# Performance work log

Measured on AMD Instinct MI355X. Metric: run time of the kernel, lower is better.

The kernel has to match this reference:

```python
import jax, jax.numpy as jnp
import numpy as np

N = 50000      # ncount
L = 4          # number of wavelet scales
E = 1600000    # nnz per sparse wavelet matrix
C_IN = 128
C_OUT = 128


def setup_inputs() -> dict:
    key = jax.random.key(0)
    ks = jax.random.split(key, 7)
    return {
        "phi_indices": jax.random.randint(ks[0], (L, 2, E), 0, N, dtype=jnp.int32),
        "phi_values": jax.random.uniform(ks[1], (L, E), dtype=jnp.float32),
        "phi_inverse_indices": jax.random.randint(ks[2], (L, 2, E), 0, N, dtype=jnp.int32),
        "phi_inverse_values": jax.random.uniform(ks[3], (L, E), dtype=jnp.float32),
        "features": jax.random.normal(ks[4], (N, L, C_IN), dtype=jnp.float32),
        "weight_matrix": jax.random.normal(ks[5], (C_IN, C_OUT), dtype=jnp.float32) * (6.0 / (C_IN + C_OUT)) ** 0.5,
        "diagonal_weight_filter": jax.random.uniform(ks[6], (N,), dtype=jnp.float32, minval=0.9, maxval=1.1),
    }


def _spmm(idx, vals, X):
    # sparse [N,N] (COO rows=idx[0], cols=idx[1]) @ dense X [N,C]
    row, col = idx[0], idx[1]
    return jax.ops.segment_sum(vals[:, None] * X[col], row, num_segments=N)


def reference(phi_indices, phi_values, phi_inverse_indices, phi_inverse_values,
              features, weight_matrix, diagonal_weight_filter):
    # Original: (phi_i @ diag(theta) @ phi_inv_i) @ (features[:,i,:] @ W)
    # Applied right-to-left via associativity -> three streaming spmm-style ops,
    # never materializing the N x N product matrix.
    def per_scale(p_idx, p_val, pi_idx, pi_val, feat_i):
        y = feat_i @ weight_matrix                 # [N, C_OUT]
        y = _spmm(pi_idx, pi_val, y)               # phi_inverse @ y
        y = y * diagonal_weight_filter[:, None]    # diag(theta) @ y
        return _spmm(p_idx, p_val, y)              # phi @ y

    feats_lf = jnp.moveaxis(features, 1, 0)        # [L, N, C_IN]
    out = jax.vmap(per_scale)(phi_indices, phi_values,
                              phi_inverse_indices, phi_inverse_values, feats_lf)
    return jnp.moveaxis(out, 0, 1)                 # [N, L, C_OUT]
```

## Files before the change

### kernel.cpp

```cpp
#include <hip/hip_runtime.h>

#define N_NODES 50000
#define L_SCALES 4
#define E_NNZ 1600000
#define C 128
#define NL (N_NODES * L_SCALES)

#define ELL_W 64
#define OVF_CAP 8192

#define RPB 16
#define NB (N_NODES / RPB)
#define NSUB 8
#define SCAP 112
#define GROUP 4
#define BT_STRIDE 16

#define SEG_SHIFT 12
#define NSEG 13

__global__ __launch_bounds__(256) void gemm_all(
    const float* __restrict__ feat,
    const float* __restrict__ W,
    float* __restrict__ Y)
{
    __shared__ float As[16][132];
    __shared__ float Ws[16][128];

    int t  = threadIdx.x;
    int ty = t >> 4;
    int tx = t & 15;
    size_t r0 = (size_t)blockIdx.x * 128;

    float acc[8][8];
    #pragma unroll
    for (int i = 0; i < 8; ++i)
        #pragma unroll
        for (int j = 0; j < 8; ++j) acc[i][j] = 0.f;

    for (int kt = 0; kt < C; kt += 16) {
        __syncthreads();
        #pragma unroll
        for (int jj = 0; jj < 2; ++jj) {
            int q = t + 256 * jj;
            int row = q >> 2, pc = q & 3;
            size_t r = r0 + row;
            float4 f = (r < (size_t)NL) ? ((const float4*)(feat + r * C + kt))[pc]
                                        : make_float4(0.f, 0.f, 0.f, 0.f);
            As[pc * 4 + 0][row] = f.x;
            As[pc * 4 + 1][row] = f.y;
            As[pc * 4 + 2][row] = f.z;
            As[pc * 4 + 3][row] = f.w;
            int kr = q >> 5, wpc = q & 31;
            ((float4*)&Ws[kr][0])[wpc] = ((const float4*)(W + (size_t)(kt + kr) * C))[wpc];
        }
        __syncthreads();

        #pragma unroll
        for (int kk = 0; kk < 16; ++kk) {
            float4 a0 = *(const float4*)&As[kk][ty * 8];
            float4 a1 = *(const float4*)&As[kk][ty * 8 + 4];
            float4 w0 = *(const float4*)&Ws[kk][tx * 4];
            float4 w1 = *(const float4*)&Ws[kk][64 + tx * 4];
            float a[8] = {a0.x, a0.y, a0.z, a0.w, a1.x, a1.y, a1.z, a1.w};
            float w[8] = {w0.x, w0.y, w0.z, w0.w, w1.x, w1.y, w1.z, w1.w};
            #pragma unroll
            for (int i = 0; i < 8; ++i)
                #pragma unroll
                for (int j = 0; j < 8; ++j)
                    acc[i][j] = fmaf(a[i], w[j], acc[i][j]);
        }
    }

    #pragma unroll
    for (int i = 0; i < 8; ++i) {
        size_t r = r0 + ty * 8 + i;
        if (r < (size_t)NL) {
            float* orow = Y + r * C;
            *(float4*)(orow + tx * 4)      = make_float4(acc[i][0], acc[i][1], acc[i][2], acc[i][3]);
            *(float4*)(orow + 64 + tx * 4) = make_float4(acc[i][4], acc[i][5], acc[i][6], acc[i][7]);
        }
    }
}

__global__ __launch_bounds__(256) void partition_edges(
    const int*   __restrict__ rows,
    const int*   __restrict__ cols,
    const float* __restrict__ vals,
    uint2* __restrict__ bkt,
    int*   __restrict__ btail,
    int* __restrict__ ovf_n, int* __restrict__ ovf_row,
    int* __restrict__ ovf_col, float* __restrict__ ovf_val)
{
    int e = blockIdx.x * 256 + threadIdx.x;
    if (e >= E_NNZ) return;
    int s = blockIdx.x & (NSUB - 1);
    int r = rows[e];
    int c = cols[e];
    float v = vals[e];
    int b = r >> 4;
    int pos = atomicAdd(&btail[(s * NB + b) * BT_STRIDE], 1);
    if (pos < SCAP) {
        bkt[((size_t)s * NB + b) * SCAP + pos] =
            make_uint2((unsigned)c | ((unsigned)(r & (RPB - 1)) << 16), __float_as_uint(v));
    } else {
        int k = atomicAdd(ovf_n, 1);
        if (k < OVF_CAP) { ovf_row[k] = r; ovf_col[k] = c; ovf_val[k] = v; }
    }
}

__global__ __launch_bounds__(256) void ell_from_buckets(
    const uint2* __restrict__ bkt,
    const int*   __restrict__ btail,
    uint2* __restrict__ ell,
    int*   __restrict__ cnt,
    int* __restrict__ ovf_n, int* __restrict__ ovf_row,
    int* __restrict__ ovf_col, float* __restrict__ ovf_val)
{
    __shared__ __align__(16) uint2 ell_s[GROUP * RPB][ELL_W];
    __shared__ int lcnt[GROUP * RPB];

    int t  = threadIdx.x;
    int b0 = blockIdx.x * GROUP;
    int r0 = b0 * RPB;

    if (t < GROUP * RPB) lcnt[t] = 0;
    __syncthreads();

    for (int g = 0; g < GROUP; ++g) {
        int b = b0 + g;
        if (b >= NB) break;
        for (int s = 0; s < NSUB; ++s) {
            int n = btail[(s * NB + b) * BT_STRIDE];
            if (n > SCAP) n = SCAP;
            for (int i = t; i < n; i += 256) {
                uint2 rec = bkt[((size_t)s * NB + b) * SCAP + i];
                int lr = g * RPB + (int)(rec.x >> 16);
                int pos = atomicAdd(&lcnt[lr], 1);
                if (pos < ELL_W) {
                    ell_s[lr][pos] = make_uint2(rec.x & 0xFFFFu, rec.y);
                } else {
                    int k = atomicAdd(ovf_n, 1);
                    if (k < OVF_CAP) {
                        ovf_row[k] = r0 + lr;
                        ovf_col[k] = (int)(rec.x & 0xFFFFu);
                        ovf_val[k] = __uint_as_float(rec.y);
                    }
                }
            }
        }
    }
    __syncthreads();

    const uint4* src = (const uint4*)&ell_s[0][0];
    for (int i = t; i < GROUP * RPB * (ELL_W / 2); i += 256) {
        int row = r0 + (i >> 5);
        if (row < N_NODES)
            ((uint4*)ell)[(size_t)row * (ELL_W / 2) + (i & 31)] = src[i];
    }
    if (t < GROUP * RPB) {
        int row = r0 + t;
        if (row < N_NODES) cnt[row] = lcnt[t];
    }
}

__global__ __launch_bounds__(256) void spmm_ell(
    const uint2* __restrict__ ell,
    const int*   __restrict__ cnt,
    const int*   __restrict__ ovf_n,
    const int*   __restrict__ ovf_row,
    const int*   __restrict__ ovf_col,
    const float* __restrict__ ovf_val,
    const float* __restrict__ X,
    const float* __restrict__ row_scale,
    float*       __restrict__ out,
    int x_stride, int out_stride)
{
    int row  = (blockIdx.x * 256 + threadIdx.x) >> 6;
    int lane = threadIdx.x & 63;

    int n   = cnt[row];
    int ncl = n < ELL_W ? n : ELL_W;

    uint2 rec = make_uint2(0u, 0u);
    if (lane < ncl) rec = ell[(size_t)row * ELL_W + lane];
    int mycol = (int)rec.x;
    int myval = (int)rec.y;
    int myseg = (lane < ncl) ? (mycol >> SEG_SHIFT) : 64;

    float2 acc = {0.f, 0.f};
    for (int s = 0; s < NSEG; ++s) {
        unsigned long long mask = __ballot(myseg == s);
        while (mask) {
            int j = __builtin_ctzll(mask);
            mask &= mask - 1;
            int   c = __builtin_amdgcn_readlane(mycol, j);
            float v = __uint_as_float((unsigned)__builtin_amdgcn_readlane(myval, j));
            float2 x = ((const float2*)(X + (size_t)c * x_stride))[lane];
            acc.x = fmaf(v, x.x, acc.x);
            acc.y = fmaf(v, x.y, acc.y);
        }
    }

    int m = *ovf_n;
    if (m > 0) {
        if (m > OVF_CAP) m = OVF_CAP;
        for (int k = 0; k < m; ++k) {
            if (ovf_row[k] == row) {
                float v = ovf_val[k];
                float2 x = ((const float2*)(X + (size_t)ovf_col[k] * x_stride))[lane];
                acc.x = fmaf(v, x.x, acc.x);
                acc.y = fmaf(v, x.y, acc.y);
            }
        }
    }

    if (row_scale) {
        float s = row_scale[row];
        acc.x *= s;
        acc.y *= s;
    }
    ((float2*)(out + (size_t)row * out_stride))[lane] = acc;
}

extern "C" void kernel_launch(void* const* d_in, const int* in_sizes, int n_in,
                              void* d_out, int out_size, void* d_ws, size_t ws_size,
                              hipStream_t stream) {
    const int*   phi_idx  = (const int*)  d_in[0];
    const float* phi_val  = (const float*)d_in[1];
    const int*   pinv_idx = (const int*)  d_in[2];
    const float* pinv_val = (const float*)d_in[3];
    const float* feat     = (const float*)d_in[4];
    const float* W        = (const float*)d_in[5];
    const float* theta    = (const float*)d_in[6];
    float* out = (float*)d_out;

    float* Z       = (float*)d_ws;
    uint2* bkt     = (uint2*)(Z + (size_t)N_NODES * C);
    uint2* ell     = bkt + (size_t)NSUB * NB * SCAP;
    int*   cnt     = (int*)(ell + (size_t)N_NODES * ELL_W);
    int*   btail   = cnt + N_NODES;
    int*   ovf_n   = btail + NSUB * NB * BT_STRIDE;
    int*   ovf_row = ovf_n + 1;
    int*   ovf_col = ovf_row + OVF_CAP;
    float* ovf_val = (float*)(ovf_col + OVF_CAP);

    dim3 blk(256);
    int gemmGrid = (NL + 127) / 128;
    int partGrid = (E_NNZ + 255) / 256;
    int ellGrid  = (NB + GROUP - 1) / GROUP;
    int spmmGrid = N_NODES * 64 / 256;

    gemm_all<<<gemmGrid, blk, 0, stream>>>(feat, W, out);

    for (int l = 0; l < L_SCALES; ++l) {
        hipMemsetAsync(btail, 0, (NSUB * NB * BT_STRIDE + 1) * sizeof(int), stream);
        partition_edges<<<partGrid, blk, 0, stream>>>(
            pinv_idx + (size_t)l * 2 * E_NNZ,
            pinv_idx + (size_t)l * 2 * E_NNZ + E_NNZ,
            pinv_val + (size_t)l * E_NNZ,
            bkt, btail, ovf_n, ovf_row, ovf_col, ovf_val);
        ell_from_buckets<<<ellGrid, blk, 0, stream>>>(
            bkt, btail, ell, cnt, ovf_n, ovf_row, ovf_col, ovf_val);
        spmm_ell<<<spmmGrid, blk, 0, stream>>>(
            ell, cnt, ovf_n, ovf_row, ovf_col, ovf_val,
            out + (size_t)l * C, theta, Z, L_SCALES * C, C);

        hipMemsetAsync(btail, 0, (NSUB * NB * BT_STRIDE + 1) * sizeof(int), stream);
        partition_edges<<<partGrid, blk, 0, stream>>>(
            phi_idx + (size_t)l * 2 * E_NNZ,
            phi_idx + (size_t)l * 2 * E_NNZ + E_NNZ,
            phi_val + (size_t)l * E_NNZ,
            bkt, btail, ovf_n, ovf_row, ovf_col, ovf_val);
        ell_from_buckets<<<ellGrid, blk, 0, stream>>>(
            bkt, btail, ell, cnt, ovf_n, ovf_row, ovf_col, ovf_val);
        spmm_ell<<<spmmGrid, blk, 0, stream>>>(
            ell, cnt, ovf_n, ovf_row, ovf_col, ovf_val,
            Z, nullptr, out + (size_t)l * C, C, L_SCALES * C);
    }
}
```

Measured before the change: 1.872 ms.

## Fuse ELL construction into the SpMM kernel and batch gather loads

Removes the separate ell_from_buckets kernel. Each SpMM block now builds its 16 rows' ELL slots in shared memory straight from the partition buckets, then computes the SpMM for those rows, so the global ELL and count arrays are never written and read back. The column-segment ballot ordering is dropped in favour of an 8-way unrolled gather that issues several X row loads before the FMAs. The trade-offs are fewer, heavier blocks and the loss of the segment-ordered access pattern that may have helped L2 locality.

```diff
diff --git a/kernel.cpp b/kernel.cpp
--- a/kernel.cpp
+++ b/kernel.cpp
@@ -13,11 +13,7 @@
 #define NB (N_NODES / RPB)
 #define NSUB 8
 #define SCAP 112
-#define GROUP 4
 #define BT_STRIDE 16
-
-#define SEG_SHIFT 12
-#define NSEG 13
 
 __global__ __launch_bounds__(256) void gemm_all(
     const float* __restrict__ feat,
@@ -109,118 +105,104 @@
     }
 }
 
-__global__ __launch_bounds__(256) void ell_from_buckets(
+__global__ __launch_bounds__(256) void spmm_fused(
     const uint2* __restrict__ bkt,
     const int*   __restrict__ btail,
-    uint2* __restrict__ ell,
-    int*   __restrict__ cnt,
     int* __restrict__ ovf_n, int* __restrict__ ovf_row,
-    int* __restrict__ ovf_col, float* __restrict__ ovf_val)
-{
-    __shared__ __align__(16) uint2 ell_s[GROUP * RPB][ELL_W];
-    __shared__ int lcnt[GROUP * RPB];
-
-    int t  = threadIdx.x;
-    int b0 = blockIdx.x * GROUP;
-    int r0 = b0 * RPB;
-
-    if (t < GROUP * RPB) lcnt[t] = 0;
-    __syncthreads();
-
-    for (int g = 0; g < GROUP; ++g) {
-        int b = b0 + g;
-        if (b >= NB) break;
-        for (int s = 0; s < NSUB; ++s) {
-            int n = btail[(s * NB + b) * BT_STRIDE];
-            if (n > SCAP) n = SCAP;
-            for (int i = t; i < n; i += 256) {
-                uint2 rec = bkt[((size_t)s * NB + b) * SCAP + i];
-                int lr = g * RPB + (int)(rec.x >> 16);
-                int pos = atomicAdd(&lcnt[lr], 1);
-                if (pos < ELL_W) {
-                    ell_s[lr][pos] = make_uint2(rec.x & 0xFFFFu, rec.y);
-                } else {
-                    int k = atomicAdd(ovf_n, 1);
-                    if (k < OVF_CAP) {
-                        ovf_row[k] = r0 + lr;
-                        ovf_col[k] = (int)(rec.x & 0xFFFFu);
-                        ovf_val[k] = __uint_as_float(rec.y);
-                    }
-                }
-            }
-        }
-    }
-    __syncthreads();
-
-    const uint4* src = (const uint4*)&ell_s[0][0];
-    for (int i = t; i < GROUP * RPB * (ELL_W / 2); i += 256) {
-        int row = r0 + (i >> 5);
-        if (row < N_NODES)
-            ((uint4*)ell)[(size_t)row * (ELL_W / 2) + (i & 31)] = src[i];
-    }
-    if (t < GROUP * RPB) {
-        int row = r0 + t;
-        if (row < N_NODES) cnt[row] = lcnt[t];
-    }
-}
-
-__global__ __launch_bounds__(256) void spmm_ell(
-    const uint2* __restrict__ ell,
-    const int*   __restrict__ cnt,
-    const int*   __restrict__ ovf_n,
-    const int*   __restrict__ ovf_row,
-    const int*   __restrict__ ovf_col,
-    const float* __restrict__ ovf_val,
+    int* __restrict__ ovf_col, float* __restrict__ ovf_val,
     const float* __restrict__ X,
     const float* __restrict__ row_scale,
     float*       __restrict__ out,
     int x_stride, int out_stride)
 {
-    int row  = (blockIdx.x * 256 + threadIdx.x) >> 6;
-    int lane = threadIdx.x & 63;
-
-    int n   = cnt[row];
-    int ncl = n < ELL_W ? n : ELL_W;
-
-    uint2 rec = make_uint2(0u, 0u);
-    if (lane < ncl) rec = ell[(size_t)row * ELL_W + lane];
-    int mycol = (int)rec.x;
-    int myval = (int)rec.y;
-    int myseg = (lane < ncl) ? (mycol >> SEG_SHIFT) : 64;
-
-    float2 acc = {0.f, 0.f};
-    for (int s = 0; s < NSEG; ++s) {
-        unsigned long long mask = __ballot(myseg == s);
-        while (mask) {
-            int j = __builtin_ctzll(mask);
-            mask &= mask - 1;
+    __shared__ __align__(16) uint2 ell_s[RPB][ELL_W];
+    __shared__ int lcnt[RPB];
+
+    int t  = threadIdx.x;
+    int b  = blockIdx.x;
+    int r0 = b * RPB;
+
+    if (t < RPB) lcnt[t] = 0;
+    __syncthreads();
+
+    for (int s = 0; s < NSUB; ++s) {
+        int n = btail[(s * NB + b) * BT_STRIDE];
+        if (n > SCAP) n = SCAP;
+        for (int i = t; i < n; i += 256) {
+            uint2 rec = bkt[((size_t)s * NB + b) * SCAP + i];
+            int lr = (int)(rec.x >> 16);
+            int pos = atomicAdd(&lcnt[lr], 1);
+            if (pos < ELL_W) {
+                ell_s[lr][pos] = make_uint2(rec.x & 0xFFFFu, rec.y);
+            } else {
+                int k = atomicAdd(ovf_n, 1);
+                if (k < OVF_CAP) {
+                    ovf_row[k] = r0 + lr;
+                    ovf_col[k] = (int)(rec.x & 0xFFFFu);
+                    ovf_val[k] = __uint_as_float(rec.y);
+                }
+            }
+        }
+    }
+    __syncthreads();
+
+    int w    = t >> 6;
+    int lane = t & 63;
+    int m = *ovf_n;
+    if (m > OVF_CAP) m = OVF_CAP;
+
+    for (int rr = 0; rr < 4; ++rr) {
+        int lr  = w * 4 + rr;
+        int row = r0 + lr;
+        int n   = lcnt[lr];
+        int ncl = n < ELL_W ? n : ELL_W;
+
+        uint2 rec = ell_s[lr][lane];
+        int mycol = (int)rec.x;
+        int myval = (int)rec.y;
+
+        float2 acc = {0.f, 0.f};
+        int j = 0;
+        for (; j + 8 <= ncl; j += 8) {
+            float2 x[8];
+            #pragma unroll
+            for (int u = 0; u < 8; ++u) {
+                int c = __builtin_amdgcn_readlane(mycol, j + u);
+                x[u] = ((const float2*)(X + (size_t)c * x_stride))[lane];
+            }
+            #pragma unroll
+            for (int u = 0; u < 8; ++u) {
+                float v = __uint_as_float((unsigned)__builtin_amdgcn_readlane(myval, j + u));
+                acc.x = fmaf(v, x[u].x, acc.x);
+                acc.y = fmaf(v, x[u].y, acc.y);
+            }
+        }
+        for (; j < ncl; ++j) {
             int   c = __builtin_amdgcn_readlane(mycol, j);
             float v = __uint_as_float((unsigned)__builtin_amdgcn_readlane(myval, j));
             float2 x = ((const float2*)(X + (size_t)c * x_stride))[lane];
             acc.x = fmaf(v, x.x, acc.x);
             acc.y = fmaf(v, x.y, acc.y);
         }
-    }
-
-    int m = *ovf_n;
-    if (m > 0) {
-        if (m > OVF_CAP) m = OVF_CAP;
-        for (int k = 0; k < m; ++k) {
-            if (ovf_row[k] == row) {
-                float v = ovf_val[k];
-                float2 x = ((const float2*)(X + (size_t)ovf_col[k] * x_stride))[lane];
-                acc.x = fmaf(v, x.x, acc.x);
-                acc.y = fmaf(v, x.y, acc.y);
-            }
-        }
-    }
-
-    if (row_scale) {
-        float s = row_scale[row];
-        acc.x *= s;
-        acc.y *= s;
-    }
-    ((float2*)(out + (size_t)row * out_stride))[lane] = acc;
+
+        if (m > 0) {
+            for (int k = 0; k < m; ++k) {
+                if (ovf_row[k] == row) {
+                    float v = ovf_val[k];
+                    float2 x = ((const float2*)(X + (size_t)ovf_col[k] * x_stride))[lane];
+                    acc.x = fmaf(v, x.x, acc.x);
+                    acc.y = fmaf(v, x.y, acc.y);
+                }
+            }
+        }
+
+        if (row_scale) {
+            float s = row_scale[row];
+            acc.x *= s;
+            acc.y *= s;
+        }
+        ((float2*)(out + (size_t)row * out_stride))[lane] = acc;
+    }
 }
 
 extern "C" void kernel_launch(void* const* d_in, const int* in_sizes, int n_in,
@@ -237,9 +219,7 @@
 
     float* Z       = (float*)d_ws;
     uint2* bkt     = (uint2*)(Z + (size_t)N_NODES * C);
-    uint2* ell     = bkt + (size_t)NSUB * NB * SCAP;
-    int*   cnt     = (int*)(ell + (size_t)N_NODES * ELL_W);
-    int*   btail   = cnt + N_NODES;
+    int*   btail   = (int*)(bkt + (size_t)NSUB * NB * SCAP);
     int*   ovf_n   = btail + NSUB * NB * BT_STRIDE;
     int*   ovf_row = ovf_n + 1;
     int*   ovf_col = ovf_row + OVF_CAP;
@@ -248,8 +228,7 @@
     dim3 blk(256);
     int gemmGrid = (NL + 127) / 128;
     int partGrid = (E_NNZ + 255) / 256;
-    int ellGrid  = (NB + GROUP - 1) / GROUP;
-    int spmmGrid = N_NODES * 64 / 256;
+    int spmmGrid = NB;
 
     gemm_all<<<gemmGrid, blk, 0, stream>>>(feat, W, out);
 
@@ -260,10 +239,8 @@
             pinv_idx + (size_t)l * 2 * E_NNZ + E_NNZ,
             pinv_val + (size_t)l * E_NNZ,
             bkt, btail, ovf_n, ovf_row, ovf_col, ovf_val);
-        ell_from_buckets<<<ellGrid, blk, 0, stream>>>(
-            bkt, btail, ell, cnt, ovf_n, ovf_row, ovf_col, ovf_val);
-        spmm_ell<<<spmmGrid, blk, 0, stream>>>(
-            ell, cnt, ovf_n, ovf_row, ovf_col, ovf_val,
+        spmm_fused<<<spmmGrid, blk, 0, stream>>>(
+            bkt, btail, ovf_n, ovf_row, ovf_col, ovf_val,
             out + (size_t)l * C, theta, Z, L_SCALES * C, C);
 
         hipMemsetAsync(btail, 0, (NSUB * NB * BT_STRIDE + 1) * sizeof(int), stream);
@@ -272,10 +249,8 @@
             phi_idx + (size_t)l * 2 * E_NNZ + E_NNZ,
             phi_val + (size_t)l * E_NNZ,
             bkt, btail, ovf_n, ovf_row, ovf_col, ovf_val);
-        ell_from_buckets<<<ellGrid, blk, 0, stream>>>(
-            bkt, btail, ell, cnt, ovf_n, ovf_row, ovf_col, ovf_val);
-        spmm_ell<<<spmmGrid, blk, 0, stream>>>(
-            ell, cnt, ovf_n, ovf_row, ovf_col, ovf_val,
+        spmm_fused<<<spmmGrid, blk, 0, stream>>>(
+            bkt, btail, ovf_n, ovf_row, ovf_col, ovf_val,
             Z, nullptr, out + (size_t)l * C, C, L_SCALES * C);
     }
 }
```

After: 1.702 ms. 9.0% less time.
